# Optimization experiments

Measured on AMD Instinct MI355X. Metric: run time of the kernel, lower is better.

The kernel has to match this reference:

```python
import jax, jax.numpy as jnp
import numpy as np

C, PH, PW, H, W = 10, 7, 7, 34, 34
STRIDE = 8.0
S = 4  # sample_per_part


def setup_inputs() -> dict:
    key = jax.random.key(0)
    k1, k2, k3, k4, k5 = jax.random.split(key, 5)
    N = 30000
    ft = jax.random.normal(k1, (1, C * PH * PW, H, W), dtype=jnp.float32)
    x1 = jax.random.uniform(k2, (N,), dtype=jnp.float32) * 200.0
    y1 = jax.random.uniform(k3, (N,), dtype=jnp.float32) * 200.0
    bw = jax.random.uniform(k4, (N,), dtype=jnp.float32) * 70.0 + 2.0
    bh = jax.random.uniform(k5, (N,), dtype=jnp.float32) * 70.0 + 2.0
    rois = jnp.stack([jnp.zeros((N,), jnp.float32), x1, y1, x1 + bw, y1 + bh], axis=1)
    return {"ft_add_left_right": ft, "rois": rois}


def reference(ft_add_left_right, rois):
    ft = ft_add_left_right[0].reshape(C, PH, PW, H, W)
    roi_start_w = rois[:, 1] / STRIDE
    roi_start_h = rois[:, 2] / STRIDE
    roi_end_w = rois[:, 3] / STRIDE
    roi_end_h = rois[:, 4] / STRIDE
    # torch.threshold(x, 0.1, 0.1): x if x > 0.1 else 0.1
    roi_height = jnp.where(roi_end_h - roi_start_h > 0.1, roi_end_h - roi_start_h, 0.1)
    roi_width = jnp.where(roi_end_w - roi_start_w > 0.1, roi_end_w - roi_start_w, 0.1)
    bin_size_h = roi_height / PH
    bin_size_w = roi_width / PW
    sub_h = bin_size_h / S
    sub_w = bin_size_w / S

    gh, gw = jnp.meshgrid(jnp.arange(PH), jnp.arange(PW), indexing='ij')
    phs = gh.reshape(-1, 1)  # [49,1]
    pws = gw.reshape(-1, 1)  # [49,1]
    hstart = jnp.floor(roi_start_h + phs * bin_size_h)  # [49,N]
    wstart = jnp.floor(roi_start_w + pws * bin_size_w)  # [49,N]

    N = rois.shape[0]
    sum_ = jnp.zeros((C, PH * PW, N), jnp.float32)
    count = jnp.zeros((PH * PW, N), jnp.float32)

    for ih in range(S):
        for iw in range(S):
            w = wstart + (iw + 0.5) * sub_w  # [49,N]
            h = hstart + (ih + 0.5) * sub_h
            keep = (w > -1) & (w < W) & (h > -1) & (h < H)
            x1 = jnp.floor(w).astype(jnp.int32)
            x2 = jnp.ceil(w).astype(jnp.int32)
            y1 = jnp.floor(h).astype(jnp.int32)
            y2 = jnp.ceil(h).astype(jnp.int32)
            x1v = (x1 >= 0) & (x1 < W)
            x2v = (x2 >= 0) & (x2 < W)
            y1v = (y1 >= 0) & (y1 < H)
            y2v = (y2 >= 0) & (y2 < H)
            x1 = jnp.clip(x1, 0, W - 1)
            x2 = jnp.clip(x2, 0, W - 1)
            y1 = jnp.clip(y1, 0, H - 1)
            y2 = jnp.clip(y2, 0, H - 1)
            dist_x = w - x1
            dist_y = h - y1
            # gathers: result [C,49,N]
            v11 = ft[:, phs, pws, y1, x1]
            v12 = ft[:, phs, pws, y2, x1]
            v21 = ft[:, phs, pws, y1, x2]
            v22 = ft[:, phs, pws, y2, x2]
            # faithful to source: ALL four masks zero value11 only (source bug)
            bad11 = (~x1v & y1v) | (~x1v & y2v) | (~x2v & y1v) | (~x2v & y2v)
            v11 = jnp.where(bad11, 0.0, v11)
            value = ((1 - dist_x) * (1 - dist_y) * v11
                     + (1 - dist_x) * dist_y * v12
                     + dist_x * (1 - dist_y) * v21
                     + dist_x * dist_y * v22)
            sum_ = sum_ + jnp.where(keep, value, 0.0)
            count = count + keep.astype(jnp.float32)

    out = jnp.where(count > 0, sum_ / jnp.maximum(count, 1.0), sum_)
    return jnp.transpose(out, (2, 0, 1))  # [N, C, 49]
```

## Files before the change

kernel.cpp:

```cpp
#include <hip/hip_runtime.h>
#include <hip/hip_fp16.h>


#define NC 10
#define NBIN 49
#define FH 34
#define FW 34
#define PLANE (FH * FW)
#define NPIX (NBIN * PLANE)
#define GPC 18882
#define RPB 16
#define TSTRIDE 491
#define NSIDE 14

__device__ __forceinline__ void pack_pixel(
    const float* __restrict__ ft, unsigned int* __restrict__ ftR, int p)
{
    unsigned int h2[5];
    if (p < NPIX) {
#pragma unroll
        for (int c = 0; c < 5; ++c) {
            const __half lo = __float2half_rn(ft[(2 * c)     * NPIX + p]);
            const __half hi = __float2half_rn(ft[(2 * c + 1) * NPIX + p]);
            const __half2 hh = __halves2half2(lo, hi);
            h2[c] = *(const unsigned int*)&hh;
        }
    } else {
#pragma unroll
        for (int c = 0; c < 5; ++c) h2[c] = 0u;
    }
#pragma unroll
    for (int m = 0; m < 3; ++m) {
        if (p >= m) {
            const int t = p - m;
            const int g = t / 3;
            const int j = t - 3 * g;
            if (g < GPC) {
                unsigned int* d = ftR + ((size_t)m * GPC + g) * 16 + j * 5;
#pragma unroll
                for (int c = 0; c < 5; ++c) d[c] = h2[c];
            }
        }
    }
}

__global__ __launch_bounds__(1024) void prep_kernel(
    const float* __restrict__ ft, unsigned int* __restrict__ ftR)
{
    const int p = blockIdx.x * 1024 + threadIdx.x;
    if (p < NPIX + 2) pack_pixel(ft, ftR, p);
}

__device__ __forceinline__ void fma2(float w, unsigned int u, float& s0, float& s1)
{
    const __half2 h = *(const __half2*)&u;
    s0 = fmaf(w, __half2float(__low2half(h)),  s0);
    s1 = fmaf(w, __half2float(__high2half(h)), s1);
}


#define BIN_META(J, EW, FP, INV, BINV, BVV)                                    \
    {                                                                          \
        BINV = (J) * RPB + s;                                                  \
        BVV = valid && (BINV < NBIN);                                          \
        const float msk = BVV ? 1.0f : 0.0f;                                   \
        const int ph = BINV / 7;                                               \
        const int pw = BINV - ph * 7;                                          \
        const float4 ya = *(const float4*)&sides[ph][r][0];                    \
        const float4 yb = *(const float4*)&sides[ph][r][4];                    \
        const float4 xa = *(const float4*)&sides[7 + pw][r][0];                \
        const float4 xb = *(const float4*)&sides[7 + pw][r][4];                \
        const float AY[3] = {ya.x, ya.y, ya.z};                                \
        const float BY[3] = {ya.w, yb.x, yb.y};                                \
        const float AX[3] = {xa.x, xa.y, xa.z};                                \
        const float BX[3] = {xa.w, xb.x, xb.y};                                \
        const int Y0 = (int)yb.w;                                              \
        const int X0 = (int)xb.w;                                              \
        const float cnt = yb.z * xb.z;                                         \
        INV = (cnt > 0.0f) ? __fdiv_rn(1.0f, cnt) : 1.0f;                      \
        const int binbase = BINV * PLANE;                                      \
        const int rowo[3] = {binbase + Y0 * FW,                                \
                             binbase + min(Y0 + 1, FH - 1) * FW,               \
                             binbase + min(Y0 + 2, FH - 1) * FW};              \
        const int e = (FW - 1) - X0;                                           \
        _Pragma("unroll") for (int p = 0; p < 3; ++p) {                        \
            const float w0 = (AY[p] * AX[0] - BY[p] * BX[0]) * msk;            \
            const float w1 = (AY[p] * AX[1] - BY[p] * BX[1]) * msk;            \
            const float w2 = (AY[p] * AX[2] - BY[p] * BX[2]) * msk;            \
            const float s12 = w1 + w2;                                         \
            EW[p][0] = (e < 1) ? (w0 + s12) : w0;                              \
            EW[p][1] = (e < 1) ? 0.f : ((e < 2) ? s12 : w1);                   \
            EW[p][2] = (e < 2) ? 0.f : w2;                                     \
            const bool rnz = (w0 != 0.0f) || (w1 != 0.0f) || (w2 != 0.0f);     \
            FP[p] = BVV ? (rnz ? (rowo[p] + X0) : binbase) : 0;                \
        }                                                                      \
    }

#define LOAD3(FP, RV)                                                          \
    _Pragma("unroll") for (int p = 0; p < 3; ++p) {                            \
        const int g = FP[p] / 3;                                               \
        const int m = FP[p] - 3 * g;                                           \
        const unsigned int* lp = ftR + ((size_t)m * GPC + g) * 16;             \
        const uint4 a = *(const uint4*)lp;                                     \
        const uint4 b4 = *(const uint4*)(lp + 4);                              \
        const uint4 c4 = *(const uint4*)(lp + 8);                              \
        const uint4 d4 = *(const uint4*)(lp + 12);                             \
        RV[p][0] = a.x;  RV[p][1] = a.y;  RV[p][2] = a.z;  RV[p][3] = a.w;     \
        RV[p][4] = b4.x; RV[p][5] = b4.y; RV[p][6] = b4.z; RV[p][7] = b4.w;    \
        RV[p][8] = c4.x; RV[p][9] = c4.y; RV[p][10] = c4.z; RV[p][11] = c4.w;  \
        RV[p][12] = d4.x; RV[p][13] = d4.y; RV[p][14] = d4.z;    \
    }

#define FMA_STORE(EW, RV, INV, BINV, BVV)                                      \
    {                                                                          \
        float sum[NC];                                                         \
        _Pragma("unroll") for (int c = 0; c < NC; ++c) sum[c] = 0.f;           \
        _Pragma("unroll") for (int p = 0; p < 3; ++p)                          \
            _Pragma("unroll") for (int c = 0; c < 5; ++c) {                    \
                fma2(EW[p][0], RV[p][c],      sum[2 * c], sum[2 * c + 1]);     \
                fma2(EW[p][1], RV[p][5 + c],  sum[2 * c], sum[2 * c + 1]);     \
                fma2(EW[p][2], RV[p][10 + c], sum[2 * c], sum[2 * c + 1]);     \
            }                                                                  \
        if (BVV) {                                                             \
            float* tp = &tile[r][0];                                           \
            _Pragma("unroll") for (int c = 0; c < NC; ++c)                     \
                tp[c * NBIN + BINV] = sum[c] * INV;                            \
        }                                                                      \
    }

__global__ __launch_bounds__(256, 3) void main_kernel(
    const float* __restrict__ rois, const unsigned int* __restrict__ ftR,
    const float* __restrict__ ft, float* __restrict__ out, int N, int use_t)
{
    __shared__ float sides[NSIDE][RPB][8];
    __shared__ float tile[RPB][TSTRIDE];

    const int r = threadIdx.x & (RPB - 1);
    const int s = threadIdx.x >> 4;
    const int n = blockIdx.x * RPB + r;
    const bool valid = (n < N);

    float rsw = 0.f, rsh = 0.f, rew = 0.f, reh = 0.f;
    if (valid) {
        rsw = rois[n * 5 + 1] * 0.125f;
        rsh = rois[n * 5 + 2] * 0.125f;
        rew = rois[n * 5 + 3] * 0.125f;
        reh = rois[n * 5 + 4] * 0.125f;
    }
    float rheight = __fsub_rn(reh, rsh);
    if (!(rheight > 0.1f)) rheight = 0.1f;
    float rwidth = __fsub_rn(rew, rsw);
    if (!(rwidth > 0.1f)) rwidth = 0.1f;
    const float bsh   = __fdiv_rn(rheight, 7.0f);
    const float bsw   = __fdiv_rn(rwidth, 7.0f);
    const float sub_h = __fdiv_rn(bsh, 4.0f);
    const float sub_w = __fdiv_rn(bsw, 4.0f);

    if (s < NSIDE) {
        const bool isY = (s < 7);
        const int  k   = isY ? s : s - 7;
        const float st = isY ? rsh : rsw;
        const float bs = isY ? bsh : bsw;
        const float sb = isY ? sub_h : sub_w;
        const float start = floorf(__fadd_rn(st, __fmul_rn((float)k, bs)));

        float A[3] = {0.f, 0.f, 0.f}, B[3] = {0.f, 0.f, 0.f};
        float cnt = 0.f;
        int P0 = 0;
#pragma unroll
        for (int i = 0; i < 4; ++i) {
            const float h = __fadd_rn(start, __fmul_rn((float)i + 0.5f, sb));
            const bool ok = (h > -1.0f) && (h < 34.0f);
            const int p1 = (int)floorf(h);
            const int p2 = (int)ceilf(h);
            const bool v1 = (p1 >= 0) && (p1 < 34);
            const bool v2 = (p2 >= 0) && (p2 < 34);
            const int p1c = min(max(p1, 0), 33);
            const int p2c = min(max(p2, 0), 33);
            const float d = __fsub_rn(h, (float)p1c);
            if (i == 0) P0 = p1c;
            const int i1 = p1c - P0, i2 = p2c - P0;
            const float t1 = ok ? (1.0f - d) : 0.0f;
            const float t2 = ok ? d : 0.0f;
            const bool bsel = isY ? (v1 || v2) : ((!v1) || (!v2));
            const float tb = (ok && bsel) ? (1.0f - d) : 0.0f;
            cnt += ok ? 1.0f : 0.0f;
#pragma unroll
            for (int p = 0; p < 3; ++p) {
                A[p] += (i1 == p) ? t1 : 0.0f;
                A[p] += (i2 == p) ? t2 : 0.0f;
                B[p] += (i1 == p) ? tb : 0.0f;
            }
        }
        float* sp = &sides[s][r][0];
        sp[0] = A[0]; sp[1] = A[1]; sp[2] = A[2];
        sp[3] = B[0]; sp[4] = B[1]; sp[5] = B[2];
        sp[6] = cnt;  sp[7] = (float)P0;
    }
    __syncthreads();

    if (use_t) {
        float ewA[3][3], ewB[3][3];
        int   fpA[3], fpB[3];
        float invA, invB;
        int   binA, binB;
        bool  bvA, bvB;
        unsigned int rvA[3][15], rvB[3][15];

        BIN_META(0, ewA, fpA, invA, binA, bvA);
        LOAD3(fpA, rvA);
        BIN_META(1, ewB, fpB, invB, binB, bvB);
        LOAD3(fpB, rvB);
        FMA_STORE(ewA, rvA, invA, binA, bvA);
        BIN_META(2, ewA, fpA, invA, binA, bvA);
        LOAD3(fpA, rvA);
        FMA_STORE(ewB, rvB, invB, binB, bvB);
        BIN_META(3, ewB, fpB, invB, binB, bvB);
        LOAD3(fpB, rvB);
        FMA_STORE(ewA, rvA, invA, binA, bvA);
        FMA_STORE(ewB, rvB, invB, binB, bvB);
    } else {
#pragma unroll
        for (int j = 0; j < 4; ++j) {
            const int bin = j * RPB + s;
            if (valid && bin < NBIN) {
                const int ph = bin / 7;
                const int pw = bin - ph * 7;
                const float4 ya = *(const float4*)&sides[ph][r][0];
                const float4 yb = *(const float4*)&sides[ph][r][4];
                const float4 xa = *(const float4*)&sides[7 + pw][r][0];
                const float4 xb = *(const float4*)&sides[7 + pw][r][4];
                const float AY[3] = {ya.x, ya.y, ya.z};
                const float BY[3] = {ya.w, yb.x, yb.y};
                const float AX[3] = {xa.x, xa.y, xa.z};
                const float BX[3] = {xa.w, xb.x, xb.y};
                const int Y0 = (int)yb.w, X0 = (int)xb.w;
                const float cnt = yb.z * xb.z;
                const int binbase = bin * PLANE;
                const int rowo[3] = {binbase + Y0 * FW,
                                     binbase + min(Y0 + 1, FH - 1) * FW,
                                     binbase + min(Y0 + 2, FH - 1) * FW};
                const int colo[3] = {X0, min(X0 + 1, FW - 1), min(X0 + 2, FW - 1)};
                float wgt[9];
                int off[9];
#pragma unroll
                for (int p = 0; p < 3; ++p)
#pragma unroll
                    for (int q2 = 0; q2 < 3; ++q2) {
                        const float w = AY[p] * AX[q2] - BY[p] * BX[q2];
                        wgt[3 * p + q2] = w;
                        off[3 * p + q2] = (w != 0.0f) ? (rowo[p] + colo[q2]) : binbase;
                    }
                float sum[NC];
#pragma unroll
                for (int c = 0; c < NC; ++c) sum[c] = 0.f;
#pragma unroll
                for (int k = 0; k < 9; ++k) {
                    const float w = wgt[k];
#pragma unroll
                    for (int c = 0; c < NC; ++c)
                        sum[c] = fmaf(w, ft[c * NPIX + off[k]], sum[c]);
                }
                const float inv = (cnt > 0.0f) ? __fdiv_rn(1.0f, cnt) : 1.0f;
                float* tp = &tile[r][0];
#pragma unroll
                for (int c = 0; c < NC; ++c) tp[c * NBIN + bin] = sum[c] * inv;
            }
        }
    }

    __syncthreads();

    const int n0 = blockIdx.x * RPB;
    for (int i = threadIdx.x; i < RPB * (NC * NBIN); i += 256) {
        const int row = i / (NC * NBIN);
        const int col = i - row * (NC * NBIN);
        const int n2 = n0 + row;
        if (n2 < N) out[(size_t)n2 * (NC * NBIN) + col] = tile[row][col];
    }
}

extern "C" void kernel_launch(void* const* d_in, const int* in_sizes, int n_in,
                              void* d_out, int out_size, void* d_ws, size_t ws_size,
                              hipStream_t stream) {
    const float* ft   = (const float*)d_in[0];
    const float* rois = (const float*)d_in[1];
    float* out        = (float*)d_out;
    const int N = in_sizes[1] / 5;

    const size_t need = (size_t)3 * GPC * 64;
    const int use_t = (ws_size >= need) ? 1 : 0;
    unsigned int* ftR = (unsigned int*)d_ws;

    if (use_t) {
        prep_kernel<<<(NPIX + 2 + 1023) / 1024, 1024, 0, stream>>>(ft, ftR);
    }
    main_kernel<<<(N + RPB - 1) / RPB, 256, 0, stream>>>(rois, ftR, ft, out, N, use_t);
}
```

Baseline: 114.3 us.

## Coalesce feature gathers via wave shuffles and LDS staging

```diff
diff --git a/kernel.cpp b/kernel.cpp
--- a/kernel.cpp
+++ b/kernel.cpp
@@ -12,6 +12,7 @@
 #define RPB 16
 #define TSTRIDE 491
 #define NSIDE 14
+#define SLOTW 20
 
 __device__ __forceinline__ void pack_pixel(
     const float* __restrict__ ft, unsigned int* __restrict__ ftR, int p)
@@ -57,7 +58,6 @@
     s0 = fmaf(w, __half2float(__low2half(h)),  s0);
     s1 = fmaf(w, __half2float(__high2half(h)), s1);
 }
-
 
 #define BIN_META(J, EW, FP, INV, BINV, BVV)                                    \
     {                                                                          \
@@ -96,44 +96,13 @@
         }                                                                      \
     }
 
-#define LOAD3(FP, RV)                                                          \
-    _Pragma("unroll") for (int p = 0; p < 3; ++p) {                            \
-        const int g = FP[p] / 3;                                               \
-        const int m = FP[p] - 3 * g;                                           \
-        const unsigned int* lp = ftR + ((size_t)m * GPC + g) * 16;             \
-        const uint4 a = *(const uint4*)lp;                                     \
-        const uint4 b4 = *(const uint4*)(lp + 4);                              \
-        const uint4 c4 = *(const uint4*)(lp + 8);                              \
-        const uint4 d4 = *(const uint4*)(lp + 12);                             \
-        RV[p][0] = a.x;  RV[p][1] = a.y;  RV[p][2] = a.z;  RV[p][3] = a.w;     \
-        RV[p][4] = b4.x; RV[p][5] = b4.y; RV[p][6] = b4.z; RV[p][7] = b4.w;    \
-        RV[p][8] = c4.x; RV[p][9] = c4.y; RV[p][10] = c4.z; RV[p][11] = c4.w;  \
-        RV[p][12] = d4.x; RV[p][13] = d4.y; RV[p][14] = d4.z;    \
-    }
-
-#define FMA_STORE(EW, RV, INV, BINV, BVV)                                      \
-    {                                                                          \
-        float sum[NC];                                                         \
-        _Pragma("unroll") for (int c = 0; c < NC; ++c) sum[c] = 0.f;           \
-        _Pragma("unroll") for (int p = 0; p < 3; ++p)                          \
-            _Pragma("unroll") for (int c = 0; c < 5; ++c) {                    \
-                fma2(EW[p][0], RV[p][c],      sum[2 * c], sum[2 * c + 1]);     \
-                fma2(EW[p][1], RV[p][5 + c],  sum[2 * c], sum[2 * c + 1]);     \
-                fma2(EW[p][2], RV[p][10 + c], sum[2 * c], sum[2 * c + 1]);     \
-            }                                                                  \
-        if (BVV) {                                                             \
-            float* tp = &tile[r][0];                                           \
-            _Pragma("unroll") for (int c = 0; c < NC; ++c)                     \
-                tp[c * NBIN + BINV] = sum[c] * INV;                            \
-        }                                                                      \
-    }
-
-__global__ __launch_bounds__(256, 3) void main_kernel(
+__global__ __launch_bounds__(256, 2) void main_kernel(
     const float* __restrict__ rois, const unsigned int* __restrict__ ftR,
     const float* __restrict__ ft, float* __restrict__ out, int N, int use_t)
 {
     __shared__ float sides[NSIDE][RPB][8];
     __shared__ float tile[RPB][TSTRIDE];
+    __shared__ unsigned int stage[4][64 * SLOTW];
 
     const int r = threadIdx.x & (RPB - 1);
     const int s = threadIdx.x >> 4;
@@ -200,25 +169,63 @@
     __syncthreads();
 
     if (use_t) {
-        float ewA[3][3], ewB[3][3];
-        int   fpA[3], fpB[3];
-        float invA, invB;
-        int   binA, binB;
-        bool  bvA, bvB;
-        unsigned int rvA[3][15], rvB[3][15];
-
-        BIN_META(0, ewA, fpA, invA, binA, bvA);
-        LOAD3(fpA, rvA);
-        BIN_META(1, ewB, fpB, invB, binB, bvB);
-        LOAD3(fpB, rvB);
-        FMA_STORE(ewA, rvA, invA, binA, bvA);
-        BIN_META(2, ewA, fpA, invA, binA, bvA);
-        LOAD3(fpA, rvA);
-        FMA_STORE(ewB, rvB, invB, binB, bvB);
-        BIN_META(3, ewB, fpB, invB, binB, bvB);
-        LOAD3(fpB, rvB);
-        FMA_STORE(ewA, rvA, invA, binA, bvA);
-        FMA_STORE(ewB, rvB, invB, binB, bvB);
+        const int L = threadIdx.x & 63;
+        unsigned int* sw = &stage[threadIdx.x >> 6][0];
+#pragma unroll
+        for (int j = 0; j < 4; ++j) {
+            float ew[3][3];
+            int   fp[3];
+            float inv;
+            int   binv;
+            bool  bvv;
+            BIN_META(j, ew, fp, inv, binv, bvv);
+
+            int adw[3];
+#pragma unroll
+            for (int p = 0; p < 3; ++p) {
+                const int g = fp[p] / 3;
+                const int m = fp[p] - 3 * g;
+                adw[p] = (m * GPC + g) * 16;
+            }
+
+            float sum[NC];
+#pragma unroll
+            for (int c = 0; c < NC; ++c) sum[c] = 0.f;
+
+#pragma unroll
+            for (int p = 0; p < 3; ++p) {
+#pragma unroll
+                for (int i = 0; i < 4; ++i) {
+                    const int src = i * 16 + (L >> 2);
+                    const int a   = __shfl(adw[p], src, 64);
+                    const uint4 v = *(const uint4*)(ftR + a + (L & 3) * 4);
+                    const int dst = src * SLOTW + 4 * ((L & 3) ^ ((src >> 3) & 3));
+                    *(uint4*)(sw + dst) = v;
+                }
+                unsigned int rv[16];
+#pragma unroll
+                for (int k = 0; k < 4; ++k) {
+                    const int rd = L * SLOTW + 4 * (k ^ ((L >> 3) & 3));
+                    const uint4 u = *(const uint4*)(sw + rd);
+                    rv[4 * k]     = u.x;
+                    rv[4 * k + 1] = u.y;
+                    rv[4 * k + 2] = u.z;
+                    rv[4 * k + 3] = u.w;
+                }
+#pragma unroll
+                for (int c = 0; c < 5; ++c) {
+                    fma2(ew[p][0], rv[c],      sum[2 * c], sum[2 * c + 1]);
+                    fma2(ew[p][1], rv[5 + c],  sum[2 * c], sum[2 * c + 1]);
+                    fma2(ew[p][2], rv[10 + c], sum[2 * c], sum[2 * c + 1]);
+                }
+            }
+
+            if (bvv) {
+                float* tp = &tile[r][0];
+#pragma unroll
+                for (int c = 0; c < NC; ++c) tp[c * NBIN + binv] = sum[c] * inv;
+            }
+        }
     } else {
 #pragma unroll
         for (int j = 0; j < 4; ++j) {
```

After: 122.6 us. 1.07x slower.

## Split packed feature layout into per-pixel uint4 plus shifted fifth-channel arrays

Applied to the files above, without the earlier changes.

```diff
diff --git a/kernel.cpp b/kernel.cpp
--- a/kernel.cpp
+++ b/kernel.cpp
@@ -8,47 +8,28 @@
 #define FW 34
 #define PLANE (FH * FW)
 #define NPIX (NBIN * PLANE)
-#define GPC 18882
 #define RPB 16
 #define TSTRIDE 491
 #define NSIDE 14
 
-__device__ __forceinline__ void pack_pixel(
-    const float* __restrict__ ft, unsigned int* __restrict__ ftR, int p)
-{
-    unsigned int h2[5];
-    if (p < NPIX) {
-#pragma unroll
-        for (int c = 0; c < 5; ++c) {
-            const __half lo = __float2half_rn(ft[(2 * c)     * NPIX + p]);
-            const __half hi = __float2half_rn(ft[(2 * c + 1) * NPIX + p]);
-            const __half2 hh = __halves2half2(lo, hi);
-            h2[c] = *(const unsigned int*)&hh;
-        }
-    } else {
-#pragma unroll
-        for (int c = 0; c < 5; ++c) h2[c] = 0u;
-    }
-#pragma unroll
-    for (int m = 0; m < 3; ++m) {
-        if (p >= m) {
-            const int t = p - m;
-            const int g = t / 3;
-            const int j = t - 3 * g;
-            if (g < GPC) {
-                unsigned int* d = ftR + ((size_t)m * GPC + g) * 16 + j * 5;
-#pragma unroll
-                for (int c = 0; c < 5; ++c) d[c] = h2[c];
-            }
-        }
-    }
-}
-
 __global__ __launch_bounds__(1024) void prep_kernel(
-    const float* __restrict__ ft, unsigned int* __restrict__ ftR)
+    const float* __restrict__ ft, unsigned int* __restrict__ ws)
 {
     const int p = blockIdx.x * 1024 + threadIdx.x;
-    if (p < NPIX + 2) pack_pixel(ft, ftR, p);
+    if (p >= NPIX) return;
+    unsigned int h2[5];
+#pragma unroll
+    for (int c = 0; c < 5; ++c) {
+        const __half lo = __float2half_rn(ft[(2 * c)     * NPIX + p]);
+        const __half hi = __float2half_rn(ft[(2 * c + 1) * NPIX + p]);
+        const __half2 hh = __halves2half2(lo, hi);
+        h2[c] = *(const unsigned int*)&hh;
+    }
+    *(uint4*)(ws + (size_t)p * 4) = make_uint4(h2[0], h2[1], h2[2], h2[3]);
+    unsigned int* fb = ws + (size_t)NPIX * 4;
+#pragma unroll
+    for (int m = 0; m < 4; ++m)
+        if (p >= m) fb[(size_t)m * NPIX + (p - m)] = h2[m == 0 ? 4 : 4];
 }
 
 __device__ __forceinline__ void fma2(float w, unsigned int u, float& s0, float& s1)
@@ -59,7 +40,7 @@
 }
 
 
-#define BIN_META(J, EW, FP, INV, BINV, BVV)                                    \
+#define BIN_META9(J, WGT, OFF, FPB, E, INV, BINV, BVV)                         \
     {                                                                          \
         BINV = (J) * RPB + s;                                                  \
         BVV = valid && (BINV < NBIN);                                          \
@@ -82,45 +63,51 @@
         const int rowo[3] = {binbase + Y0 * FW,                                \
                              binbase + min(Y0 + 1, FH - 1) * FW,               \
                              binbase + min(Y0 + 2, FH - 1) * FW};              \
-        const int e = (FW - 1) - X0;                                           \
+        const int colo[3] = {X0, min(X0 + 1, FW - 1), min(X0 + 2, FW - 1)};    \
+        E = (FW - 1) - X0;                                                     \
         _Pragma("unroll") for (int p = 0; p < 3; ++p) {                        \
-            const float w0 = (AY[p] * AX[0] - BY[p] * BX[0]) * msk;            \
-            const float w1 = (AY[p] * AX[1] - BY[p] * BX[1]) * msk;            \
-            const float w2 = (AY[p] * AX[2] - BY[p] * BX[2]) * msk;            \
-            const float s12 = w1 + w2;                                         \
-            EW[p][0] = (e < 1) ? (w0 + s12) : w0;                              \
-            EW[p][1] = (e < 1) ? 0.f : ((e < 2) ? s12 : w1);                   \
-            EW[p][2] = (e < 2) ? 0.f : w2;                                     \
-            const bool rnz = (w0 != 0.0f) || (w1 != 0.0f) || (w2 != 0.0f);     \
-            FP[p] = BVV ? (rnz ? (rowo[p] + X0) : binbase) : 0;                \
-        }                                                                      \
-    }
-
-#define LOAD3(FP, RV)                                                          \
-    _Pragma("unroll") for (int p = 0; p < 3; ++p) {                            \
-        const int g = FP[p] / 3;                                               \
-        const int m = FP[p] - 3 * g;                                           \
-        const unsigned int* lp = ftR + ((size_t)m * GPC + g) * 16;             \
-        const uint4 a = *(const uint4*)lp;                                     \
-        const uint4 b4 = *(const uint4*)(lp + 4);                              \
-        const uint4 c4 = *(const uint4*)(lp + 8);                              \
-        const uint4 d4 = *(const uint4*)(lp + 12);                             \
-        RV[p][0] = a.x;  RV[p][1] = a.y;  RV[p][2] = a.z;  RV[p][3] = a.w;     \
-        RV[p][4] = b4.x; RV[p][5] = b4.y; RV[p][6] = b4.z; RV[p][7] = b4.w;    \
-        RV[p][8] = c4.x; RV[p][9] = c4.y; RV[p][10] = c4.z; RV[p][11] = c4.w;  \
-        RV[p][12] = d4.x; RV[p][13] = d4.y; RV[p][14] = d4.z;    \
-    }
-
-#define FMA_STORE(EW, RV, INV, BINV, BVV)                                      \
+            bool rnz = false;                                                  \
+            _Pragma("unroll") for (int q = 0; q < 3; ++q) {                    \
+                const float w = (AY[p] * AX[q] - BY[p] * BX[q]) * msk;         \
+                WGT[3 * p + q] = w;                                            \
+                OFF[3 * p + q] =                                               \
+                    BVV ? ((w != 0.0f) ? (rowo[p] + colo[q]) : binbase) : 0;   \
+                rnz = rnz || (w != 0.0f);                                      \
+            }                                                                  \
+            FPB[p] = BVV ? (rnz ? (rowo[p] + X0) : binbase) : 0;               \
+        }                                                                      \
+    }
+
+#define LOAD9(OFF, FPB, VA, VB)                                                \
+    {                                                                          \
+        _Pragma("unroll") for (int k = 0; k < 9; ++k)                          \
+            VA[k] = *(const uint4*)(ftH + (size_t)OFF[k] * 4);                 \
+        _Pragma("unroll") for (int p = 0; p < 3; ++p) {                        \
+            const int m = FPB[p] & 3;                                          \
+            const int i0 = FPB[p] & ~3;                                        \
+            VB[p] = *(const uint4*)(fB + (size_t)m * NPIX + i0);               \
+        }                                                                      \
+    }
+
+#define FMA_STORE9(WGT, E, VA, VB, INV, BINV, BVV)                             \
     {                                                                          \
         float sum[NC];                                                         \
         _Pragma("unroll") for (int c = 0; c < NC; ++c) sum[c] = 0.f;           \
-        _Pragma("unroll") for (int p = 0; p < 3; ++p)                          \
-            _Pragma("unroll") for (int c = 0; c < 5; ++c) {                    \
-                fma2(EW[p][0], RV[p][c],      sum[2 * c], sum[2 * c + 1]);     \
-                fma2(EW[p][1], RV[p][5 + c],  sum[2 * c], sum[2 * c + 1]);     \
-                fma2(EW[p][2], RV[p][10 + c], sum[2 * c], sum[2 * c + 1]);     \
-            }                                                                  \
+        _Pragma("unroll") for (int k = 0; k < 9; ++k) {                        \
+            const float w = WGT[k];                                            \
+            fma2(w, VA[k].x, sum[0], sum[1]);                                  \
+            fma2(w, VA[k].y, sum[2], sum[3]);                                  \
+            fma2(w, VA[k].z, sum[4], sum[5]);                                  \
+            fma2(w, VA[k].w, sum[6], sum[7]);                                  \
+        }                                                                      \
+        _Pragma("unroll") for (int p = 0; p < 3; ++p) {                        \
+            const unsigned int u0 = VB[p].x;                                   \
+            const unsigned int u1 = (E >= 1) ? VB[p].y : VB[p].x;              \
+            const unsigned int u2 = (E >= 2) ? VB[p].z : u1;                   \
+            fma2(WGT[3 * p + 0], u0, sum[8], sum[9]);                          \
+            fma2(WGT[3 * p + 1], u1, sum[8], sum[9]);                          \
+            fma2(WGT[3 * p + 2], u2, sum[8], sum[9]);                          \
+        }                                                                      \
         if (BVV) {                                                             \
             float* tp = &tile[r][0];                                           \
             _Pragma("unroll") for (int c = 0; c < NC; ++c)                     \
@@ -129,7 +116,7 @@
     }
 
 __global__ __launch_bounds__(256, 3) void main_kernel(
-    const float* __restrict__ rois, const unsigned int* __restrict__ ftR,
+    const float* __restrict__ rois, const unsigned int* __restrict__ ftH,
     const float* __restrict__ ft, float* __restrict__ out, int N, int use_t)
 {
     __shared__ float sides[NSIDE][RPB][8];
@@ -200,25 +187,28 @@
     __syncthreads();
 
     if (use_t) {
-        float ewA[3][3], ewB[3][3];
-        int   fpA[3], fpB[3];
+        const unsigned int* fB = ftH + (size_t)NPIX * 4;
+        float wgtA[9], wgtB[9];
+        int   offA[9], offB[9];
+        int   fpbA[3], fpbB[3];
+        int   eA, eB, binA, binB;
         float invA, invB;
-        int   binA, binB;
         bool  bvA, bvB;
-        unsigned int rvA[3][15], rvB[3][15];
-
-        BIN_META(0, ewA, fpA, invA, binA, bvA);
-        LOAD3(fpA, rvA);
-        BIN_META(1, ewB, fpB, invB, binB, bvB);
-        LOAD3(fpB, rvB);
-        FMA_STORE(ewA, rvA, invA, binA, bvA);
-        BIN_META(2, ewA, fpA, invA, binA, bvA);
-        LOAD3(fpA, rvA);
-        FMA_STORE(ewB, rvB, invB, binB, bvB);
-        BIN_META(3, ewB, fpB, invB, binB, bvB);
-        LOAD3(fpB, rvB);
-        FMA_STORE(ewA, rvA, invA, binA, bvA);
-        FMA_STORE(ewB, rvB, invB, binB, bvB);
+        uint4 vaA[9], vaB[9];
+        uint4 vbA[3], vbB[3];
+
+        BIN_META9(0, wgtA, offA, fpbA, eA, invA, binA, bvA);
+        LOAD9(offA, fpbA, vaA, vbA);
+        BIN_META9(1, wgtB, offB, fpbB, eB, invB, binB, bvB);
+        LOAD9(offB, fpbB, vaB, vbB);
+        FMA_STORE9(wgtA, eA, vaA, vbA, invA, binA, bvA);
+        BIN_META9(2, wgtA, offA, fpbA, eA, invA, binA, bvA);
+        LOAD9(offA, fpbA, vaA, vbA);
+        FMA_STORE9(wgtB, eB, vaB, vbB, invB, binB, bvB);
+        BIN_META9(3, wgtB, offB, fpbB, eB, invB, binB, bvB);
+        LOAD9(offB, fpbB, vaB, vbB);
+        FMA_STORE9(wgtA, eA, vaA, vbA, invA, binA, bvA);
+        FMA_STORE9(wgtB, eB, vaB, vbB, invB, binB, bvB);
     } else {
 #pragma unroll
         for (int j = 0; j < 4; ++j) {
@@ -288,12 +278,12 @@
     float* out        = (float*)d_out;
     const int N = in_sizes[1] / 5;
 
-    const size_t need = (size_t)3 * GPC * 64;
+    const size_t need = (size_t)NPIX * 16 + (size_t)4 * NPIX * 4;
     const int use_t = (ws_size >= need) ? 1 : 0;
-    unsigned int* ftR = (unsigned int*)d_ws;
+    unsigned int* ftH = (unsigned int*)d_ws;
 
     if (use_t) {
-        prep_kernel<<<(NPIX + 2 + 1023) / 1024, 1024, 0, stream>>>(ft, ftR);
-    }
-    main_kernel<<<(N + RPB - 1) / RPB, 256, 0, stream>>>(rois, ftR, ft, out, N, use_t);
-}
+        prep_kernel<<<(NPIX + 1023) / 1024, 1024, 0, stream>>>(ft, ftH);
+    }
+    main_kernel<<<(N + RPB - 1) / RPB, 256, 0, stream>>>(rois, ftH, ft, out, N, use_t);
+}
```

After: 109.3 us. 4.4% less time.
